# Performance work log

Hardware: AMD Instinct MI355X
Metric: run time of the kernel (lower is better)

The kernel has to match this reference:

```python
import jax, jax.numpy as jnp
import numpy as np

N = 4096        # nodes == batch_size (GFN operates on dense N x N adjacency)
E = 65536       # edges per view (avg degree 16)
IN = 512        # per-view input feature dim
HV = [128, 64]  # per-view GCN dims
HM = [64, 64]   # fused-graph GCN dims
VIEWS = 3


def setup_inputs() -> dict:
    key = jax.random.key(0)
    ks = iter(jax.random.split(key, 64))

    def xavier(shape):
        lim = float(np.sqrt(6.0 / (shape[0] + shape[1])))
        return jax.random.uniform(next(ks), shape, minval=-lim, maxval=lim, dtype=jnp.float32)

    inp = {}
    for v in range(VIEWS):
        inp[f"x{v}"] = jax.random.normal(next(ks), (N, IN), dtype=jnp.float32)
        inp[f"src{v}"] = jax.random.randint(next(ks), (E,), 0, N, dtype=jnp.int32)
        inp[f"dst{v}"] = jax.random.randint(next(ks), (E,), 0, N, dtype=jnp.int32)
        inp[f"Wv{v}0"] = xavier((IN, HV[0]))
        inp[f"bv{v}0"] = jnp.zeros((HV[0],), jnp.float32)
        inp[f"Wv{v}1"] = xavier((HV[0], HV[1]))
        inp[f"bv{v}1"] = jnp.zeros((HV[1],), jnp.float32)
        inp[f"Wf{v}"] = xavier((HV[1], HV[1]))  # FeatureFusion weight
    # GFN: Linear(N -> N/2) -> ReLU -> Linear(N/2 -> N)
    inp["Wg1"] = xavier((N, N // 2)); inp["bg1"] = jnp.zeros((N // 2,), jnp.float32)
    inp["Wg2"] = xavier((N // 2, N)); inp["bg2"] = jnp.zeros((N,), jnp.float32)
    # fused-graph GCN layers
    inp["Wm0"] = xavier((HV[1], HM[0])); inp["bm0"] = jnp.zeros((HM[0],), jnp.float32)
    inp["Wm1"] = xavier((HM[0], HM[1])); inp["bm1"] = jnp.zeros((HM[1],), jnp.float32)
    return inp


def _deg_norms(src, dst):
    # DGL GraphConv norm='both': scale by out-deg(src)^-1/2 and in-deg(dst)^-1/2, degrees clamped to >=1
    ones = jnp.ones(src.shape[0], jnp.float32)
    dout = jnp.maximum(jax.ops.segment_sum(ones, src, num_segments=N), 1.0)
    din = jnp.maximum(jax.ops.segment_sum(ones, dst, num_segments=N), 1.0)
    return dout ** -0.5, din ** -0.5


def _gconv(x, W, b, src, dst, do_isqrt, di_isqrt, act):
    h = (x * do_isqrt[:, None]) @ W            # [N, out] (W commutes with row scaling)
    agg = jax.ops.segment_sum(h[src], dst, num_segments=N)
    h = agg * di_isqrt[:, None] + b
    return act(h)


def reference(x0, x1, x2, src0, dst0, src1, dst1, src2, dst2,
              Wv00, bv00, Wv01, bv01, Wv10, bv10, Wv11, bv11, Wv20, bv20, Wv21, bv21,
              Wf0, Wf1, Wf2, Wg1, bg1, Wg2, bg2, Wm0, bm0, Wm1, bm1):
    ident = lambda t: t
    xs = [x0, x1, x2]
    edges = [(src0, dst0), (src1, dst1), (src2, dst2)]
    Wv = [(Wv00, bv00, Wv01, bv01), (Wv10, bv10, Wv11, bv11), (Wv20, bv20, Wv21, bv21)]
    Wf = [Wf0, Wf1, Wf2]

    # per-view GCN stacks (relu on first layer, identity on last)
    feats = []
    for v in range(VIEWS):
        src, dst = edges[v]
        do_i, di_i = _deg_norms(src, dst)
        W0, b0, W1, b1 = Wv[v]
        f = _gconv(xs[v], W0, b0, src, dst, do_i, di_i, jax.nn.relu)
        f = _gconv(f, W1, b1, src, dst, do_i, di_i, ident)
        feats.append(f)

    # FeatureFusion (dropout omitted for determinism): sum(f @ Wf), softmax over features, relu
    z = feats[0] @ Wf[0] + feats[1] @ Wf[1] + feats[2] @ Wf[2]
    z = jax.nn.relu(jax.nn.softmax(z, axis=1))

    # consensus graph: sum of per-view dense adjacencies -> GFN -> clamp -> round(+0.1)
    adj = jnp.zeros((N, N), jnp.float32)
    for src, dst in edges:
        adj = adj + jnp.zeros((N, N), jnp.float32).at[src, dst].set(1.0)
    fused = jax.nn.relu(adj @ Wg1 + bg1) @ Wg2 + bg2
    fused = jnp.round(jnp.clip(fused, 0.0, 1.0) + 0.1)
    adj_r = fused

    # rebuild binary graph (went through numpy in original -> stop_gradient), symmetrize, add self-loops
    sym = jax.lax.stop_gradient(fused)
    sym = sym + sym.T
    A = jnp.maximum((sym > 0).astype(jnp.float32), jnp.eye(N, dtype=jnp.float32))
    deg = A.sum(axis=1)
    dn = deg ** -0.5

    # fused-graph GCN layers (dense normalized SpMM form since A is already dense)
    h = z
    h = jax.nn.relu(((A @ (h * dn[:, None])) * dn[:, None]) @ Wm0 + bm0)
    h = ((A @ (h * dn[:, None])) * dn[:, None]) @ Wm1 + bm1

    # InnerProductDecoder with identity activation; all `views` entries of adj_rec are identical
    adj_rec = h @ h.T
    return (adj_r, adj_rec, h)
```

## Files before the change

kernel.cpp:

```cpp
#include <hip/hip_runtime.h>
#include <math.h>

#define NNODES 4096
#define NEDGES 65536

typedef short bf16x8 __attribute__((ext_vector_type(8)));
typedef short short4v __attribute__((ext_vector_type(4)));
typedef float f32x4 __attribute__((ext_vector_type(4)));
typedef float f32x4v __attribute__((ext_vector_type(4)));

struct Ptr3  { const float* p[3]; };
struct Ptr3i { const int*   p[3]; };
struct Ptr3h { const short* p[3]; };

__device__ __forceinline__ short f2bf(float f) {
    unsigned u = __builtin_bit_cast(unsigned, f);
    unsigned r = (u + 0x7FFFu + ((u >> 16) & 1u)) >> 16;
    return (short)r;
}

__device__ __forceinline__ void gload_lds16(const void* g, void* l) {
    __builtin_amdgcn_global_load_lds(
        (const __attribute__((address_space(1))) unsigned*)g,
        (__attribute__((address_space(3))) unsigned*)l, 16, 0, 0);
}

template<int ACT>
__global__ __launch_bounds__(512, 1)
void gm_k(const short* __restrict__ A, const short* __restrict__ Bt,
          const float* __restrict__ bias, void* __restrict__ Cout, float* __restrict__ Cout1,
          unsigned char* __restrict__ Pout, int M, int Nn, int K, int lda, int ldb)
{
    constexpr int SLOT = 32768;
    __shared__ short lds[2 * SLOT];
    const int tid = threadIdx.x;
    const int lane = tid & 63;
    const int wave = tid >> 6;
    const int wm = wave >> 2, wn = wave & 3;
    const int z = blockIdx.z;
    A  += (size_t)z * K;
    Bt += (size_t)z * K;
    float* Cf = (ACT == 3 && z == 1) ? Cout1 : (float*)Cout;
    const int gx = gridDim.x, nwg = gx * gridDim.y;
    int w = blockIdx.y * gx + blockIdx.x;
    const int q8 = nwg >> 3;
    w = (w & 7) * q8 + (w >> 3);
    const int bm0 = (w / gx) * 256, bn0 = (w % gx) * 256;
    const int NT = K >> 6;

    auto stageH = [&](int t, int part) {
        if (t >= NT) return;
        const int k0 = t << 6;
        char* base = (char*)(lds + (t & 1) * SLOT);
        const int isB = (part < 2);
        const int h = part & 1;
#pragma unroll
        for (int r = 0; r < 2; ++r) {
            int o = r * 8192 + tid * 16;
            int row = o >> 7;
            int grow = h * 128 + row;
            int scol = (((o >> 4) & 7) ^ (grow & 7)) << 3;
            const short* gsrc = isB ? (Bt + (size_t)(bn0 + grow) * ldb + k0 + scol)
                                    : (A  + (size_t)(bm0 + grow) * lda + k0 + scol);
            gload_lds16(gsrc, base + (isB ? 32768 : 0) + h * 16384 + r * 8192 + wave * 1024);
        }
    };

    f32x4 acc[8][4] = {};
    bf16x8 aF[4][2];
    bf16x8 bF[4][2];

#define PH(QM, QN, TCUR, T1, P1, T2, P2, VM)                                          \
    {                                                                                 \
        const short* As_ = lds + ((TCUR) & 1) * SLOT;                                 \
        const short* Bs_ = As_ + 16384;                                               \
        if constexpr ((QN) == 0) {                                                    \
            _Pragma("unroll") for (int kk = 0; kk < 2; ++kk) {                        \
                const int h_ = kk * 4 + (lane >> 4);                                  \
                _Pragma("unroll") for (int i = 0; i < 4; ++i) {                       \
                    int r_ = wm * 128 + (QM) * 64 + i * 16 + (lane & 15);             \
                    aF[i][kk] = *(const bf16x8*)(As_ + r_ * 64 + ((h_ ^ (r_ & 7)) << 3)); \
                }                                                                     \
            }                                                                         \
        }                                                                             \
        if constexpr ((QM) == 0) {                                                    \
            _Pragma("unroll") for (int kk = 0; kk < 2; ++kk) {                        \
                const int h_ = kk * 4 + (lane >> 4);                                  \
                _Pragma("unroll") for (int j = 0; j < 2; ++j) {                       \
                    int r_ = wn * 64 + ((QN) * 2 + j) * 16 + (lane & 15);             \
                    bF[(QN) * 2 + j][kk] = *(const bf16x8*)(Bs_ + r_ * 64 + ((h_ ^ (r_ & 7)) << 3)); \
                }                                                                     \
            }                                                                         \
        }                                                                             \
        if ((P1) >= 0) stageH(T1, P1);                                                \
        if ((P2) >= 0) stageH(T2, P2);                                                \
        __builtin_amdgcn_s_barrier();                                                 \
        __builtin_amdgcn_s_setprio(1);                                                \
        _Pragma("unroll") for (int kk = 0; kk < 2; ++kk)                              \
            _Pragma("unroll") for (int i = 0; i < 4; ++i)                             \
                _Pragma("unroll") for (int j = 0; j < 2; ++j)                         \
                    acc[(QM) * 4 + i][(QN) * 2 + j] =                                 \
                        __builtin_amdgcn_mfma_f32_16x16x32_bf16(                      \
                            aF[i][kk], bF[(QN) * 2 + j][kk],                          \
                            acc[(QM) * 4 + i][(QN) * 2 + j], 0, 0, 0);                \
        __builtin_amdgcn_s_setprio(0);                                                \
        if ((VM) == 6)      { asm volatile("s_waitcnt vmcnt(6)" ::: "memory");        \
                              __builtin_amdgcn_sched_barrier(0); }                    \
        else if ((VM) == 0) { asm volatile("s_waitcnt vmcnt(0)" ::: "memory");        \
                              __builtin_amdgcn_sched_barrier(0); }                    \
        __builtin_amdgcn_s_barrier();                                                 \
    }

    stageH(0, 0); stageH(0, 1); stageH(0, 2); stageH(0, 3);
    if (NT > 1) { stageH(1, 0); stageH(1, 1); stageH(1, 2); }
    if (NT > 1) { asm volatile("s_waitcnt vmcnt(6)" ::: "memory"); }
    else        { asm volatile("s_waitcnt vmcnt(0)" ::: "memory"); }
    __builtin_amdgcn_sched_barrier(0);
    __builtin_amdgcn_s_barrier();

    for (int it = 0; it < NT / 2; ++it) {
        const int t0 = 2 * it, t1 = t0 + 1, t2 = t0 + 2, t3 = t0 + 3;
        const int vm4 = (t2 < NT) ? 6 : 0;
        const int vm8 = (t3 < NT) ? 6 : 0;
        PH(0, 0, t0, t1, 3,  0, -1, -1)
        PH(0, 1, t0,  0, -1, 0, -1, -1)
        PH(1, 0, t0, t2, 0, t2,  1, -1)
        PH(1, 1, t0, t2, 2,  0, -1, vm4)
        PH(0, 0, t1, t2, 3,  0, -1, -1)
        PH(0, 1, t1,  0, -1, 0, -1, -1)
        PH(1, 0, t1, t3, 0, t3,  1, -1)
        PH(1, 1, t1, t3, 2,  0, -1, vm8)
    }
    if (NT & 1) {
        const int tl = NT - 1;
        PH(0, 0, tl, 0, -1, 0, -1, -1)
        PH(0, 1, tl, 0, -1, 0, -1, -1)
        PH(1, 0, tl, 0, -1, 0, -1, -1)
        PH(1, 1, tl, 0, -1, 0, -1, -1)
    }
#undef PH

    const int cr = (lane >> 4) * 4;
    const int cc = lane & 15;
#pragma unroll
    for (int im = 0; im < 8; ++im) {
#pragma unroll
        for (int jn = 0; jn < 4; ++jn) {
            int col = bn0 + wn * 64 + jn * 16 + cc;
            float bv = bias ? bias[col] : 0.f;
#pragma unroll
            for (int q2 = 0; q2 < 4; ++q2) {
                int row = bm0 + wm * 128 + (im >> 2) * 64 + (im & 3) * 16 + cr + q2;
                float v = acc[im][jn][q2] + bv;
                if constexpr (ACT == 2) {
                    v = rintf(fminf(fmaxf(v, 0.f), 1.f) + 0.1f);
                    Cf[(size_t)row * Nn + col] = v;
                    Pout[(size_t)row * Nn + col] = (unsigned char)(v > 0.5f);
                } else {
                    Cf[(size_t)row * Nn + col] = v;
                }
            }
        }
    }
}

__global__ void reduce_h1_k(const float* __restrict__ p0, const float* __restrict__ p1,
                            const float* __restrict__ bias, short* __restrict__ H1b)
{
    int i = (blockIdx.x * 256 + threadIdx.x) * 4;
    f32x4v a = *(const f32x4v*)(p0 + i);
    f32x4v b = *(const f32x4v*)(p1 + i);
    int col = i & 2047;
    short4v o;
#pragma unroll
    for (int j = 0; j < 4; ++j) {
        float v = a[j] + b[j] + bias[col + j];
        o[j] = f2bf(fmaxf(v, 0.f));
    }
    *(short4v*)(H1b + i) = o;
}

__global__ __launch_bounds__(256)
void mfma_gemm_b_k(const short* __restrict__ Aall, Ptr3h Btv, float* __restrict__ Call,
                   int M, int Nn, int K)
{
    __shared__ short As[64 * 64];
    __shared__ short Bs[64 * 64];
    const int z = blockIdx.z;
    const short* A = Aall + (size_t)z * M * K;
    const short* Bt = Btv.p[z];
    float* C = Call + (size_t)z * M * Nn;
    const int tid = threadIdx.x;
    const int lane = tid & 63, wave = tid >> 6;
    const int bm0 = blockIdx.y * 64, bn0 = blockIdx.x * 64;
    const int wr = (wave >> 1) * 32, wc = (wave & 1) * 32;

    f32x4 acc[2][2] = {};

    for (int k0 = 0; k0 < K; k0 += 64) {
        for (int c = wave; c < 8; c += 4) {
            int o = c * 1024 + lane * 16;
            int row = o >> 7;
            int sl = (o >> 4) & 7;
            int ss = sl ^ (row & 7);
            gload_lds16(A + ((size_t)(bm0 + row) * K + k0 + ss * 8), As + c * 512);
            gload_lds16(Bt + ((size_t)(bn0 + row) * K + k0 + ss * 8), Bs + c * 512);
        }
        __syncthreads();
#pragma unroll
        for (int kk = 0; kk < 2; ++kk) {
            bf16x8 a[2], b[2];
            const int khalf = kk * 4 + (lane >> 4);
#pragma unroll
            for (int i = 0; i < 2; ++i) {
                int r = wr + i * 16 + (lane & 15);
                a[i] = *(const bf16x8*)(As + r * 64 + ((khalf ^ (r & 7)) << 3));
            }
#pragma unroll
            for (int j = 0; j < 2; ++j) {
                int r = wc + j * 16 + (lane & 15);
                b[j] = *(const bf16x8*)(Bs + r * 64 + ((khalf ^ (r & 7)) << 3));
            }
#pragma unroll
            for (int i = 0; i < 2; ++i)
#pragma unroll
                for (int j = 0; j < 2; ++j)
                    acc[i][j] = __builtin_amdgcn_mfma_f32_16x16x32_bf16(a[i], b[j], acc[i][j], 0, 0, 0);
        }
        __syncthreads();
    }

    const int cr = (lane >> 4) * 4;
    const int cc = lane & 15;
#pragma unroll
    for (int i = 0; i < 2; ++i)
#pragma unroll
        for (int j = 0; j < 2; ++j)
#pragma unroll
            for (int q = 0; q < 4; ++q) {
                int row = bm0 + wr + i * 16 + cr + q;
                int col = bn0 + wc + j * 16 + cc;
                C[(size_t)row * Nn + col] = acc[i][j][q];
            }
}

__global__ __launch_bounds__(256)
void spmm_mfma_k(const short* __restrict__ A2b, const short* __restrict__ XsT,
                 float* __restrict__ part)
{
    __shared__ short As[64 * 64];
    __shared__ short Bs[128 * 64];
    const int tid = threadIdx.x;
    const int lane = tid & 63, wave = tid >> 6;
    const int kc = blockIdx.x, m0 = blockIdx.y * 64;
    const int wr = (wave >> 1) * 32, wc = (wave & 1) * 32;
    const int woff = wave * 512;

    f32x4 acc[2][2] = {};

    for (int k0 = kc * 512; k0 < kc * 512 + 512; k0 += 64) {
#pragma unroll
        for (int r = 0; r < 2; ++r) {
            int o = r * 4096 + tid * 16;
            int row = o >> 7;
            int sl = (o >> 4) & 7;
            gload_lds16(A2b + ((size_t)(m0 + row) * 4096 + k0 + ((sl ^ (row & 7)) << 3)),
                        As + r * 2048 + woff);
        }
#pragma unroll
        for (int r = 0; r < 4; ++r) {
            int o = r * 4096 + tid * 16;
            int row = o >> 7;
            int sl = (o >> 4) & 7;
            gload_lds16(XsT + ((size_t)row * 4096 + k0 + ((sl ^ (row & 7)) << 3)),
                        Bs + r * 2048 + woff);
        }
        __syncthreads();
#pragma unroll
        for (int kk = 0; kk < 2; ++kk) {
            const int h = kk * 4 + (lane >> 4);
            bf16x8 a[2], bh[2], bl[2];
#pragma unroll
            for (int i = 0; i < 2; ++i) {
                int r = wr + i * 16 + (lane & 15);
                a[i] = *(const bf16x8*)(As + r * 64 + ((h ^ (r & 7)) << 3));
            }
#pragma unroll
            for (int j = 0; j < 2; ++j) {
                int r = wc + j * 16 + (lane & 15);
                bh[j] = *(const bf16x8*)(Bs + r * 64 + ((h ^ (r & 7)) << 3));
                int r2 = r + 64;
                bl[j] = *(const bf16x8*)(Bs + r2 * 64 + ((h ^ (r2 & 7)) << 3));
            }
#pragma unroll
            for (int i = 0; i < 2; ++i)
#pragma unroll
                for (int j = 0; j < 2; ++j) {
                    acc[i][j] = __builtin_amdgcn_mfma_f32_16x16x32_bf16(a[i], bh[j], acc[i][j], 0, 0, 0);
                    acc[i][j] = __builtin_amdgcn_mfma_f32_16x16x32_bf16(a[i], bl[j], acc[i][j], 0, 0, 0);
                }
        }
        __syncthreads();
    }

    const int cr = (lane >> 4) * 4;
    const int cc = lane & 15;
#pragma unroll
    for (int i = 0; i < 2; ++i)
#pragma unroll
        for (int j = 0; j < 2; ++j)
#pragma unroll
            for (int q = 0; q < 4; ++q)
                part[((size_t)kc * NNODES + m0 + wr + i * 16 + cr + q) * 64 + wc + j * 16 + cc]
                    = acc[i][j][q];
}

__global__ void xsT_k(const float* __restrict__ X, const int* __restrict__ degA,
                      short* __restrict__ XsT)
{
    const int n = blockIdx.y;
    const int k = blockIdx.x * 256 + threadIdx.x;
    float v = X[(size_t)k * 64 + n] * (1.0f / sqrtf((float)degA[k]));
    short hi = f2bf(v);
    float hif = __builtin_bit_cast(float, ((unsigned)(unsigned short)hi) << 16);
    short lo = f2bf(v - hif);
    XsT[(size_t)n * 4096 + k] = hi;
    XsT[(size_t)(64 + n) * 4096 + k] = lo;
}

__global__ void a2b_k(const unsigned* __restrict__ A8w, short* __restrict__ A2b, int words)
{
    int t = blockIdx.x * 256 + threadIdx.x;
    if (t < words) {
        unsigned w = A8w[t];
        short4v o;
#pragma unroll
        for (int j = 0; j < 4; ++j) o[j] = ((w >> (8 * j)) & 1u) ? (short)0x3F80 : (short)0;
        *(short4v*)(A2b + (size_t)t * 4) = o;
    }
}

__global__ void f32_to_bf16T_k(const float* __restrict__ src, short* __restrict__ dstT,
                               int R, int C)
{
    __shared__ float t[64][65];
    const int br = blockIdx.y * 64, bc = blockIdx.x * 64;
    for (int idx = threadIdx.x; idx < 64 * 64; idx += 256) {
        int r = idx >> 6, c = idx & 63;
        t[r][c] = src[(size_t)(br + r) * C + bc + c];
    }
    __syncthreads();
    for (int idx = threadIdx.x; idx < 64 * 64; idx += 256) {
        int c = idx >> 6, r = idx & 63;
        dstT[(size_t)(bc + c) * R + br + r] = f2bf(t[r][c]);
    }
}

__global__ void mask_to_bf16_k(const unsigned* __restrict__ mask, short* __restrict__ adj,
                               int words)
{
    int t = blockIdx.x * 256 + threadIdx.x;
    if (t < words) {
        unsigned w = mask[t];
        short4v o;
        o.x = f2bf((float)__popc(w & 0x7u));
        o.y = f2bf((float)__popc(w & 0x700u));
        o.z = f2bf((float)__popc(w & 0x70000u));
        o.w = f2bf((float)__popc(w & 0x7000000u));
        *(short4v*)(adj + (size_t)t * 4) = o;
    }
}

__global__ void xsplit_k(Ptr3 xv, const float* __restrict__ isq, short* __restrict__ xe)
{
    const int z = blockIdx.y;
    int t = blockIdx.x * 256 + threadIdx.x;
    int n = t >> 9, k = t & 511;
    float a = xv.p[z][(size_t)n * 512 + k] * isq[2 * z * NNODES + n];
    short hi = f2bf(a);
    float hif = __builtin_bit_cast(float, ((unsigned)(unsigned short)hi) << 16);
    short lo = f2bf(a - hif);
    short* row = xe + (size_t)z * NNODES * 1536 + (size_t)n * 1536;
    row[k] = hi; row[512 + k] = hi; row[1024 + k] = lo;
}

__global__ void wsplitT_k(Ptr3 Wv, short* __restrict__ out, int K, int Nn)
{
    const int z = blockIdx.y;
    int t = blockIdx.x * 256 + threadIdx.x;
    if (t >= K * Nn) return;
    int k = t / Nn, n = t % Nn;
    float w = Wv.p[z][(size_t)k * Nn + n];
    short hi = f2bf(w);
    float hif = __builtin_bit_cast(float, ((unsigned)(unsigned short)hi) << 16);
    short lo = f2bf(w - hif);
    short* row = out + (size_t)z * Nn * 3 * K + (size_t)n * 3 * K;
    row[k] = hi; row[K + k] = lo; row[2 * K + k] = hi;
}

template<int RELU>
__global__ __launch_bounds__(256)
void redgemm_k(const float* __restrict__ part, const int* __restrict__ degA,
               const float* __restrict__ Wm, const float* __restrict__ bias,
               float* __restrict__ out, short* __restrict__ Ae, short* __restrict__ Be)
{
    __shared__ float Ws[64 * 64];
    const int tid = threadIdx.x;
    for (int i = tid; i < 4096; i += 256) Ws[i] = Wm[i];
    __syncthreads();
    const int lane = tid & 63, wave = tid >> 6;
    const float bv = bias[lane];
    for (int rr = 0; rr < 4; ++rr) {
        int row = blockIdx.x * 16 + wave * 4 + rr;
        float s = 0.f;
#pragma unroll
        for (int p = 0; p < 8; ++p) s += part[((size_t)p * NNODES + row) * 64 + lane];
        s *= 1.0f / sqrtf((float)degA[row]);
        float acc = bv;
#pragma unroll
        for (int k = 0; k < 64; ++k)
            acc = fmaf(__shfl(s, k), Ws[k * 64 + lane], acc);
        if (RELU) acc = fmaxf(acc, 0.f);
        out[(size_t)row * 64 + lane] = acc;
        if (Ae) {
            short hi = f2bf(acc);
            float hif = __builtin_bit_cast(float, ((unsigned)(unsigned short)hi) << 16);
            short lo = f2bf(acc - hif);
            size_t ro = (size_t)row * 192;
            Ae[ro + lane] = hi; Ae[ro + 64 + lane] = hi; Ae[ro + 128 + lane] = lo;
            Be[ro + lane] = hi; Be[ro + 64 + lane] = lo; Be[ro + 128 + lane] = hi;
        }
    }
}

__global__ void edge_k(Ptr3i src, Ptr3i dst, unsigned* __restrict__ mask, int* __restrict__ degs)
{
    int e = blockIdx.x * 256 + threadIdx.x;
    int z = blockIdx.y;
    if (e < NEDGES) {
        int s = src.p[z][e], d = dst.p[z][e];
        unsigned c = (unsigned)s * (unsigned)NNODES + (unsigned)d;
        atomicOr(&mask[c >> 2], 1u << ((c & 3u) * 8u + (unsigned)z));
        atomicAdd(&degs[2 * z * NNODES + s], 1);
        atomicAdd(&degs[(2 * z + 1) * NNODES + d], 1);
    }
}

__global__ void deg_norm_k(const int* __restrict__ degs, float* __restrict__ isq, int n)
{
    int t = blockIdx.x * 256 + threadIdx.x;
    if (t < n) isq[t] = 1.0f / sqrtf(fmaxf((float)degs[t], 1.0f));
}

__global__ __launch_bounds__(1024)
void scan_k(const int* __restrict__ degs, int* __restrict__ rowptr, int* __restrict__ cursor)
{
    const int z = blockIdx.x;
    const int* din = degs + (2 * z + 1) * NNODES;
    __shared__ int sm[1024];
    const int t = threadIdx.x;
    int v0 = din[t * 4], v1 = din[t * 4 + 1], v2 = din[t * 4 + 2], v3 = din[t * 4 + 3];
    int c1 = v0 + v1, c2 = c1 + v2, s = c2 + v3;
    sm[t] = s;
    __syncthreads();
    for (int off = 1; off < 1024; off <<= 1) {
        int add = (t >= off) ? sm[t - off] : 0;
        __syncthreads();
        sm[t] += add;
        __syncthreads();
    }
    int base = sm[t] - s;
    int* rp = rowptr + z * NNODES;
    int* cu = cursor + z * NNODES;
    rp[t * 4] = base;          cu[t * 4] = base;
    rp[t * 4 + 1] = base + v0; cu[t * 4 + 1] = base + v0;
    rp[t * 4 + 2] = base + c1; cu[t * 4 + 2] = base + c1;
    rp[t * 4 + 3] = base + c2; cu[t * 4 + 3] = base + c2;
}

__global__ void fill_k(Ptr3i src, Ptr3i dst, int* __restrict__ cursor, int* __restrict__ eidx)
{
    int e = blockIdx.x * 256 + threadIdx.x;
    int z = blockIdx.y;
    if (e < NEDGES) {
        int d = dst.p[z][e];
        int pos = atomicAdd(&cursor[z * NNODES + d], 1);
        eidx[(size_t)z * NEDGES + pos] = src.p[z][e];
    }
}

template<int F, int ACT, int MODE>
__global__ void gather_k(const float* __restrict__ Hpre, const int* __restrict__ eidx,
                         const int* __restrict__ rowptr, const int* __restrict__ degs,
                         const float* __restrict__ isq, Ptr3 bias, short* __restrict__ Sout)
{
    const int z = blockIdx.y;
    const int tid = threadIdx.x;
    const int node = blockIdx.x * (256 / F) + tid / F;
    const int f = tid % F;
    const float* H = Hpre + (size_t)z * NNODES * F;
    const int base = rowptr[z * NNODES + node];
    const int cnt = degs[(2 * z + 1) * NNODES + node];
    const int* ei = eidx + (size_t)z * NEDGES + base;
    float s = 0.f;
    for (int i = 0; i < cnt; ++i) s += H[(size_t)ei[i] * F + f];
    float v = s * isq[(2 * z + 1) * NNODES + node] + bias.p[z][f];
    if (ACT) v = fmaxf(v, 0.f);
    if (MODE == 1) v *= isq[2 * z * NNODES + node];
    short hi = f2bf(v);
    float hif = __builtin_bit_cast(float, ((unsigned)(unsigned short)hi) << 16);
    short lo = f2bf(v - hif);
    short* row = Sout + (size_t)z * NNODES * 3 * F + (size_t)node * 3 * F;
    row[f] = hi; row[F + f] = hi; row[2 * F + f] = lo;
}

__global__ void softsum_k(const float* __restrict__ zp, float* __restrict__ z)
{
    int row = blockIdx.x * 4 + (threadIdx.x >> 6);
    int f = threadIdx.x & 63;
    size_t i = (size_t)row * 64 + f;
    float v = zp[i] + zp[i + (size_t)NNODES * 64] + zp[i + (size_t)2 * NNODES * 64];
    float m = v;
#pragma unroll
    for (int off = 32; off >= 1; off >>= 1) m = fmaxf(m, __shfl_xor(m, off));
    float e = expf(v - m);
    float s = e;
#pragma unroll
    for (int off = 32; off >= 1; off >>= 1) s += __shfl_xor(s, off);
    z[i] = e / s;
}

__global__ __launch_bounds__(256)
void build_A2_k(const unsigned char* __restrict__ P, unsigned char* __restrict__ A8,
                int* __restrict__ degA)
{
    __shared__ unsigned Ts[64][20];
    const int bi = blockIdx.y * 64, bj = blockIdx.x * 64;
    const int tid = threadIdx.x;
    const int r = tid >> 2, seg = tid & 3;
    uint4 tv = *(const uint4*)(P + (size_t)(bj + r) * NNODES + bi + seg * 16);
    Ts[r][seg * 4 + 0] = tv.x; Ts[r][seg * 4 + 1] = tv.y;
    Ts[r][seg * 4 + 2] = tv.z; Ts[r][seg * 4 + 3] = tv.w;
    __syncthreads();
    uint4 dv = *(const uint4*)(P + (size_t)(bi + r) * NNODES + bj + seg * 16);
    unsigned dw[4] = {dv.x, dv.y, dv.z, dv.w};
    const unsigned char* Tb = (const unsigned char*)Ts;
    unsigned ow[4];
    int psum = 0;
#pragma unroll
    for (int w = 0; w < 4; ++w) {
        unsigned o = 0;
#pragma unroll
        for (int b = 0; b < 4; ++b) {
            int j = seg * 16 + w * 4 + b;
            unsigned a = (dw[w] >> (8 * b)) & 1u;
            unsigned tr = Tb[j * 80 + r] & 1u;
            unsigned on = a | tr | (unsigned)((bi + r) == (bj + j));
            o |= on << (8 * b);
            psum += (int)on;
        }
        ow[w] = o;
    }
    uint4 o4; o4.x = ow[0]; o4.y = ow[1]; o4.z = ow[2]; o4.w = ow[3];
    *(uint4*)(A8 + (size_t)(bi + r) * NNODES + bj + seg * 16) = o4;
    psum += __shfl_xor(psum, 1);
    psum += __shfl_xor(psum, 2);
    if (seg == 0) atomicAdd(&degA[bi + r], psum);
}

extern "C" void kernel_launch(void* const* d_in, const int* in_sizes, int n_in,
                              void* d_out, int out_size, void* d_ws, size_t ws_size,
                              hipStream_t stream)
{
    const int N = NNODES, E = NEDGES;
    const size_t MB = 1024 * 1024;

    const float* x[3]; const int* src[3]; const int* dst[3];
    const float *Wv0[3], *bv0[3], *Wv1[3], *bv1[3], *Wf[3];
    for (int v = 0; v < 3; ++v) {
        const int b = v * 8;
        x[v]   = (const float*)d_in[b + 0];
        src[v] = (const int*)  d_in[b + 1];
        dst[v] = (const int*)  d_in[b + 2];
        Wv0[v] = (const float*)d_in[b + 3];
        bv0[v] = (const float*)d_in[b + 4];
        Wv1[v] = (const float*)d_in[b + 5];
        bv1[v] = (const float*)d_in[b + 6];
        Wf[v]  = (const float*)d_in[b + 7];
    }
    const float* Wg1 = (const float*)d_in[24];
    const float* bg1 = (const float*)d_in[25];
    const float* Wg2 = (const float*)d_in[26];
    const float* bg2 = (const float*)d_in[27];
    const float* Wm0 = (const float*)d_in[28];
    const float* bm0 = (const float*)d_in[29];
    const float* Wm1 = (const float*)d_in[30];
    const float* bm1 = (const float*)d_in[31];

    float* out_adjr = (float*)d_out;
    float* out_rec  = out_adjr + (size_t)N * N;
    float* out_h    = out_rec + (size_t)N * N;

    char* oa = (char*)out_adjr;
    short* AdjB = (short*)oa;
    float* hv1  = (float*)(oa + 32 * MB);
    short* Ae2  = (short*)(oa + 38 * MB);
    short* Ae3  = (short*)(oa + 47 * MB);
    float* hv2  = (float*)(oa + 52 * MB);
    float* zp   = (float*)(oa + 56 * MB);
    float* partg0 = (float*)(oa + 32 * MB);

    char* orc = (char*)out_rec;
    short* xe   = (short*)orc;
    short* H1b  = (short*)orc;
    unsigned char* P = (unsigned char*)(orc + 16 * MB);
    short* Wg1T = (short*)(orc + 16 * MB);
    float* partg1 = (float*)(orc + 32 * MB);
    short* Wg2T = (short*)(orc + 32 * MB);
    short* A2b  = (short*)orc;
    float* part = (float*)(orc + 48 * MB);

    char* p = (char*)d_ws;
    unsigned* mask = (unsigned*)p;
    unsigned char* A8 = (unsigned char*)p;
    short* AeF = (short*)p;
    short* BeF = AeF + (size_t)N * 192;
    p += (size_t)N * N;
    int* degs = (int*)p;     p += (size_t)6 * N * 4;
    float* isq = (float*)p;  p += (size_t)6 * N * 4;
    int* rowptr = (int*)p;   p += (size_t)3 * N * 4;
    int* cursor = (int*)p;   p += (size_t)3 * N * 4;
    int* eidx = (int*)p;     p += (size_t)3 * E * 4;
    int* degA = (int*)p;     p += (size_t)N * 4;
    float* zbuf = (float*)p; p += (size_t)N * 64 * 4;
    float* h1m = (float*)p;  p += (size_t)N * 64 * 4;
    short* XsT = (short*)p;  p += (size_t)128 * N * 2;
    short* Wv0T = (short*)p; p += (size_t)3 * 128 * 1536 * 2;
    short* Wv1T = (short*)p; p += (size_t)3 * 64 * 384 * 2;
    short* WfT  = (short*)p; p += (size_t)3 * 64 * 192 * 2;

    Ptr3i srcP, dstP;
    for (int v = 0; v < 3; ++v) { srcP.p[v] = src[v]; dstP.p[v] = dst[v]; }

    hipMemsetAsync(mask, 0, (size_t)N * N, stream);
    hipMemsetAsync(degs, 0, (size_t)6 * N * 4, stream);

    edge_k<<<dim3((E + 255) / 256, 3), 256, 0, stream>>>(srcP, dstP, mask, degs);
    deg_norm_k<<<(6 * N + 255) / 256, 256, 0, stream>>>(degs, isq, 6 * N);
    scan_k<<<3, 1024, 0, stream>>>(degs, rowptr, cursor);
    fill_k<<<dim3((E + 255) / 256, 3), 256, 0, stream>>>(srcP, dstP, cursor, eidx);

    Ptr3 xP; for (int v = 0; v < 3; ++v) xP.p[v] = x[v];
    xsplit_k<<<dim3(N * 512 / 256, 3), 256, 0, stream>>>(xP, isq, xe);
    Ptr3 wP;
    for (int v = 0; v < 3; ++v) wP.p[v] = Wv0[v];
    wsplitT_k<<<dim3(512 * 128 / 256, 3), 256, 0, stream>>>(wP, Wv0T, 512, 128);
    for (int v = 0; v < 3; ++v) wP.p[v] = Wv1[v];
    wsplitT_k<<<dim3(128 * 64 / 256, 3), 256, 0, stream>>>(wP, Wv1T, 128, 64);
    for (int v = 0; v < 3; ++v) wP.p[v] = Wf[v];
    wsplitT_k<<<dim3(64 * 64 / 256, 3), 256, 0, stream>>>(wP, WfT, 64, 64);

    Ptr3h BtP; Ptr3 biasP;
    for (int v = 0; v < 3; ++v) BtP.p[v] = Wv0T + (size_t)v * 128 * 1536;
    mfma_gemm_b_k<<<dim3(2, N / 64, 3), 256, 0, stream>>>(xe, BtP, hv1, N, 128, 1536);
    for (int v = 0; v < 3; ++v) biasP.p[v] = bv0[v];
    gather_k<128, 1, 1><<<dim3(N / 2, 3), 256, 0, stream>>>(hv1, eidx, rowptr, degs, isq, biasP, Ae2);
    for (int v = 0; v < 3; ++v) BtP.p[v] = Wv1T + (size_t)v * 64 * 384;
    mfma_gemm_b_k<<<dim3(1, N / 64, 3), 256, 0, stream>>>(Ae2, BtP, hv2, N, 64, 384);
    for (int v = 0; v < 3; ++v) biasP.p[v] = bv1[v];
    gather_k<64, 0, 2><<<dim3(N / 4, 3), 256, 0, stream>>>(hv2, eidx, rowptr, degs, isq, biasP, Ae3);
    for (int v = 0; v < 3; ++v) BtP.p[v] = WfT + (size_t)v * 64 * 192;
    mfma_gemm_b_k<<<dim3(1, N / 64, 3), 256, 0, stream>>>(Ae3, BtP, zp, N, 64, 192);
    softsum_k<<<N / 4, 256, 0, stream>>>(zp, zbuf);

    mask_to_bf16_k<<<(N * N / 4 + 255) / 256, 256, 0, stream>>>(mask, AdjB, N * N / 4);
    f32_to_bf16T_k<<<dim3(2048 / 64, 4096 / 64), 256, 0, stream>>>(Wg1, Wg1T, 4096, 2048);

    gm_k<3><<<dim3(2048 / 256, 4096 / 256, 2), 512, 0, stream>>>(
        AdjB, Wg1T, nullptr, partg0, partg1, nullptr, 4096, 2048, 2048, 4096, 4096);
    reduce_h1_k<<<4096 * 2048 / 4 / 256, 256, 0, stream>>>(partg0, partg1, bg1, H1b);

    f32_to_bf16T_k<<<dim3(4096 / 64, 2048 / 64), 256, 0, stream>>>(Wg2, Wg2T, 2048, 4096);

    gm_k<2><<<dim3(4096 / 256, 4096 / 256, 1), 512, 0, stream>>>(
        H1b, Wg2T, bg2, out_adjr, nullptr, P, 4096, 4096, 2048, 2048, 2048);

    hipMemsetAsync(degA, 0, (size_t)N * 4, stream);
    build_A2_k<<<dim3(N / 64, N / 64), 256, 0, stream>>>(P, A8, degA);

    a2b_k<<<(N * N / 4 + 255) / 256, 256, 0, stream>>>((const unsigned*)A8, A2b, N * N / 4);
    xsT_k<<<dim3(16, 64), 256, 0, stream>>>(zbuf, degA, XsT);
    spmm_mfma_k<<<dim3(8, N / 64), 256, 0, stream>>>(A2b, XsT, part);
    redgemm_k<1><<<256, 256, 0, stream>>>(part, degA, Wm0, bm0, h1m, nullptr, nullptr);
    xsT_k<<<dim3(16, 64), 256, 0, stream>>>(h1m, degA, XsT);
    spmm_mfma_k<<<dim3(8, N / 64), 256, 0, stream>>>(A2b, XsT, part);
    redgemm_k<0><<<256, 256, 0, stream>>>(part, degA, Wm1, bm1, out_h, AeF, BeF);

    gm_k<0><<<dim3(4096 / 256, 4096 / 256, 1), 512, 0, stream>>>(
        AeF, BeF, nullptr, out_rec, nullptr, nullptr, 4096, 4096, 192, 192, 192);
}
```

Baseline: 452.8 us.

## Store GFN split-K partials as bf16 and fuse the adjacency and XsT conversion kernels

The split-K partial sums of the first GFN GEMM are now written as bf16 rather than fp32, which halves the traffic into and out of the reduce kernel. build_A2 writes the bf16 adjacency directly, so the separate byte-mask to bf16 conversion pass is gone. redgemm now emits the scaled hi/lo XsT for the next SpMM, replacing a second xsT launch. The changes also add an lgkmcnt wait in the GEMM phase and move the Wg2 transpose earlier. Rounding the partials to bf16 adds error before the ReLU and round/clip step, which could flip thresholded adjacency entries.

```diff
diff --git a/kernel.cpp b/kernel.cpp
--- a/kernel.cpp
+++ b/kernel.cpp
@@ -7,7 +7,6 @@
 typedef short bf16x8 __attribute__((ext_vector_type(8)));
 typedef short short4v __attribute__((ext_vector_type(4)));
 typedef float f32x4 __attribute__((ext_vector_type(4)));
-typedef float f32x4v __attribute__((ext_vector_type(4)));
 
 struct Ptr3  { const float* p[3]; };
 struct Ptr3i { const int*   p[3]; };
@@ -18,6 +17,9 @@
     unsigned r = (u + 0x7FFFu + ((u >> 16) & 1u)) >> 16;
     return (short)r;
 }
+__device__ __forceinline__ float bf2f(short s) {
+    return __builtin_bit_cast(float, ((unsigned)(unsigned short)s) << 16);
+}
 
 __device__ __forceinline__ void gload_lds16(const void* g, void* l) {
     __builtin_amdgcn_global_load_lds(
@@ -28,7 +30,7 @@
 template<int ACT>
 __global__ __launch_bounds__(512, 1)
 void gm_k(const short* __restrict__ A, const short* __restrict__ Bt,
-          const float* __restrict__ bias, void* __restrict__ Cout, float* __restrict__ Cout1,
+          const float* __restrict__ bias, void* __restrict__ Cout, void* __restrict__ Cout1,
           unsigned char* __restrict__ Pout, int M, int Nn, int K, int lda, int ldb)
 {
     constexpr int SLOT = 32768;
@@ -40,7 +42,7 @@
     const int z = blockIdx.z;
     A  += (size_t)z * K;
     Bt += (size_t)z * K;
-    float* Cf = (ACT == 3 && z == 1) ? Cout1 : (float*)Cout;
+    void* Cw = (ACT == 3 && z == 1) ? Cout1 : Cout;
     const int gx = gridDim.x, nwg = gx * gridDim.y;
     int w = blockIdx.y * gx + blockIdx.x;
     const int q8 = nwg >> 3;
@@ -94,6 +96,9 @@
         }                                                                             \
         if ((P1) >= 0) stageH(T1, P1);                                                \
         if ((P2) >= 0) stageH(T2, P2);                                                \
+        if constexpr ((QM) == 0 && (QN) == 0) {                                       \
+            asm volatile("s_waitcnt lgkmcnt(8)" ::: "memory");                        \
+        }                                                                             \
         __builtin_amdgcn_s_barrier();                                                 \
         __builtin_amdgcn_s_setprio(1);                                                \
         _Pragma("unroll") for (int kk = 0; kk < 2; ++kk)                              \
@@ -154,30 +159,32 @@
                 float v = acc[im][jn][q2] + bv;
                 if constexpr (ACT == 2) {
                     v = rintf(fminf(fmaxf(v, 0.f), 1.f) + 0.1f);
-                    Cf[(size_t)row * Nn + col] = v;
+                    ((float*)Cw)[(size_t)row * Nn + col] = v;
                     Pout[(size_t)row * Nn + col] = (unsigned char)(v > 0.5f);
+                } else if constexpr (ACT == 3) {
+                    ((short*)Cw)[(size_t)row * Nn + col] = f2bf(v);
                 } else {
-                    Cf[(size_t)row * Nn + col] = v;
+                    ((float*)Cw)[(size_t)row * Nn + col] = v;
                 }
             }
         }
     }
 }
 
-__global__ void reduce_h1_k(const float* __restrict__ p0, const float* __restrict__ p1,
+__global__ void reduce_h1_k(const short* __restrict__ p0, const short* __restrict__ p1,
                             const float* __restrict__ bias, short* __restrict__ H1b)
 {
-    int i = (blockIdx.x * 256 + threadIdx.x) * 4;
-    f32x4v a = *(const f32x4v*)(p0 + i);
-    f32x4v b = *(const f32x4v*)(p1 + i);
+    int i = (blockIdx.x * 256 + threadIdx.x) * 8;
+    bf16x8 a = *(const bf16x8*)(p0 + i);
+    bf16x8 b = *(const bf16x8*)(p1 + i);
     int col = i & 2047;
-    short4v o;
-#pragma unroll
-    for (int j = 0; j < 4; ++j) {
-        float v = a[j] + b[j] + bias[col + j];
+    bf16x8 o;
+#pragma unroll
+    for (int j = 0; j < 8; ++j) {
+        float v = bf2f(a[j]) + bf2f(b[j]) + bias[col + j];
         o[j] = f2bf(fmaxf(v, 0.f));
     }
-    *(short4v*)(H1b + i) = o;
+    *(bf16x8*)(H1b + i) = o;
 }
 
 __global__ __launch_bounds__(256)
@@ -322,22 +329,9 @@
     const int k = blockIdx.x * 256 + threadIdx.x;
     float v = X[(size_t)k * 64 + n] * (1.0f / sqrtf((float)degA[k]));
     short hi = f2bf(v);
-    float hif = __builtin_bit_cast(float, ((unsigned)(unsigned short)hi) << 16);
-    short lo = f2bf(v - hif);
+    short lo = f2bf(v - bf2f(hi));
     XsT[(size_t)n * 4096 + k] = hi;
     XsT[(size_t)(64 + n) * 4096 + k] = lo;
-}
-
-__global__ void a2b_k(const unsigned* __restrict__ A8w, short* __restrict__ A2b, int words)
-{
-    int t = blockIdx.x * 256 + threadIdx.x;
-    if (t < words) {
-        unsigned w = A8w[t];
-        short4v o;
-#pragma unroll
-        for (int j = 0; j < 4; ++j) o[j] = ((w >> (8 * j)) & 1u) ? (short)0x3F80 : (short)0;
-        *(short4v*)(A2b + (size_t)t * 4) = o;
-    }
 }
 
 __global__ void f32_to_bf16T_k(const float* __restrict__ src, short* __restrict__ dstT,
@@ -378,8 +372,7 @@
     int n = t >> 9, k = t & 511;
     float a = xv.p[z][(size_t)n * 512 + k] * isq[2 * z * NNODES + n];
     short hi = f2bf(a);
-    float hif = __builtin_bit_cast(float, ((unsigned)(unsigned short)hi) << 16);
-    short lo = f2bf(a - hif);
+    short lo = f2bf(a - bf2f(hi));
     short* row = xe + (size_t)z * NNODES * 1536 + (size_t)n * 1536;
     row[k] = hi; row[512 + k] = hi; row[1024 + k] = lo;
 }
@@ -392,8 +385,7 @@
     int k = t / Nn, n = t % Nn;
     float w = Wv.p[z][(size_t)k * Nn + n];
     short hi = f2bf(w);
-    float hif = __builtin_bit_cast(float, ((unsigned)(unsigned short)hi) << 16);
-    short lo = f2bf(w - hif);
+    short lo = f2bf(w - bf2f(hi));
     short* row = out + (size_t)z * Nn * 3 * K + (size_t)n * 3 * K;
     row[k] = hi; row[K + k] = lo; row[2 * K + k] = hi;
 }
@@ -402,7 +394,8 @@
 __global__ __launch_bounds__(256)
 void redgemm_k(const float* __restrict__ part, const int* __restrict__ degA,
                const float* __restrict__ Wm, const float* __restrict__ bias,
-               float* __restrict__ out, short* __restrict__ Ae, short* __restrict__ Be)
+               float* __restrict__ out, short* __restrict__ Ae, short* __restrict__ Be,
+               short* __restrict__ XsT)
 {
     __shared__ float Ws[64 * 64];
     const int tid = threadIdx.x;
@@ -415,7 +408,8 @@
         float s = 0.f;
 #pragma unroll
         for (int p = 0; p < 8; ++p) s += part[((size_t)p * NNODES + row) * 64 + lane];
-        s *= 1.0f / sqrtf((float)degA[row]);
+        const float dn = 1.0f / sqrtf((float)degA[row]);
+        s *= dn;
         float acc = bv;
 #pragma unroll
         for (int k = 0; k < 64; ++k)
@@ -424,11 +418,17 @@
         out[(size_t)row * 64 + lane] = acc;
         if (Ae) {
             short hi = f2bf(acc);
-            float hif = __builtin_bit_cast(float, ((unsigned)(unsigned short)hi) << 16);
-            short lo = f2bf(acc - hif);
+            short lo = f2bf(acc - bf2f(hi));
             size_t ro = (size_t)row * 192;
             Ae[ro + lane] = hi; Ae[ro + 64 + lane] = hi; Ae[ro + 128 + lane] = lo;
             Be[ro + lane] = hi; Be[ro + 64 + lane] = lo; Be[ro + 128 + lane] = hi;
+        }
+        if (XsT) {
+            float vv = acc * dn;
+            short hi = f2bf(vv);
+            short lo = f2bf(vv - bf2f(hi));
+            XsT[(size_t)lane * 4096 + row] = hi;
+            XsT[(size_t)(64 + lane) * 4096 + row] = lo;
         }
     }
 }
@@ -449,7 +449,7 @@
 __global__ void deg_norm_k(const int* __restrict__ degs, float* __restrict__ isq, int n)
 {
     int t = blockIdx.x * 256 + threadIdx.x;
-    if (t < n) isq[t] = 1.0f / sqrtf(fmaxf((float)degs[t], 1.0f));
+    if (t < n) isq[t] = 1.0f / sqrtf(fmaxf((float)t >= 0 ? (float)degs[t] : 1.0f, 1.0f));
 }
 
 __global__ __launch_bounds__(1024)
@@ -508,8 +508,7 @@
     if (ACT) v = fmaxf(v, 0.f);
     if (MODE == 1) v *= isq[2 * z * NNODES + node];
     short hi = f2bf(v);
-    float hif = __builtin_bit_cast(float, ((unsigned)(unsigned short)hi) << 16);
-    short lo = f2bf(v - hif);
+    short lo = f2bf(v - bf2f(hi));
     short* row = Sout + (size_t)z * NNODES * 3 * F + (size_t)node * 3 * F;
     row[f] = hi; row[F + f] = hi; row[2 * F + f] = lo;
 }
@@ -531,7 +530,7 @@
 }
 
 __global__ __launch_bounds__(256)
-void build_A2_k(const unsigned char* __restrict__ P, unsigned char* __restrict__ A8,
+void build_A2_k(const unsigned char* __restrict__ P, short* __restrict__ A2b,
                 int* __restrict__ degA)
 {
     __shared__ unsigned Ts[64][20];
@@ -545,24 +544,25 @@
     uint4 dv = *(const uint4*)(P + (size_t)(bi + r) * NNODES + bj + seg * 16);
     unsigned dw[4] = {dv.x, dv.y, dv.z, dv.w};
     const unsigned char* Tb = (const unsigned char*)Ts;
-    unsigned ow[4];
+    bf16x8 o0, o1;
     int psum = 0;
 #pragma unroll
     for (int w = 0; w < 4; ++w) {
-        unsigned o = 0;
 #pragma unroll
         for (int b = 0; b < 4; ++b) {
-            int j = seg * 16 + w * 4 + b;
+            int idx = w * 4 + b;
+            int j = seg * 16 + idx;
             unsigned a = (dw[w] >> (8 * b)) & 1u;
             unsigned tr = Tb[j * 80 + r] & 1u;
             unsigned on = a | tr | (unsigned)((bi + r) == (bj + j));
-            o |= on << (8 * b);
+            short val = on ? (short)0x3F80 : (short)0;
+            if (idx < 8) o0[idx] = val; else o1[idx - 8] = val;
             psum += (int)on;
         }
-        ow[w] = o;
-    }
-    uint4 o4; o4.x = ow[0]; o4.y = ow[1]; o4.z = ow[2]; o4.w = ow[3];
-    *(uint4*)(A8 + (size_t)(bi + r) * NNODES + bj + seg * 16) = o4;
+    }
+    short* dst = A2b + (size_t)(bi + r) * NNODES + bj + seg * 16;
+    *(bf16x8*)dst = o0;
+    *(bf16x8*)(dst + 8) = o1;
     psum += __shfl_xor(psum, 1);
     psum += __shfl_xor(psum, 2);
     if (seg == 0) atomicAdd(&degA[bi + r], psum);
@@ -608,21 +608,19 @@
     short* Ae3  = (short*)(oa + 47 * MB);
     float* hv2  = (float*)(oa + 52 * MB);
     float* zp   = (float*)(oa + 56 * MB);
-    float* partg0 = (float*)(oa + 32 * MB);
+    short* partg0 = (short*)(oa + 32 * MB);
+    short* partg1 = (short*)(oa + 48 * MB);
 
     char* orc = (char*)out_rec;
     short* xe   = (short*)orc;
     short* H1b  = (short*)orc;
     unsigned char* P = (unsigned char*)(orc + 16 * MB);
     short* Wg1T = (short*)(orc + 16 * MB);
-    float* partg1 = (float*)(orc + 32 * MB);
     short* Wg2T = (short*)(orc + 32 * MB);
-    short* A2b  = (short*)orc;
     float* part = (float*)(orc + 48 * MB);
 
     char* p = (char*)d_ws;
     unsigned* mask = (unsigned*)p;
-    unsigned char* A8 = (unsigned char*)p;
     short* AeF = (short*)p;
     short* BeF = AeF + (size_t)N * 192;
     p += (size_t)N * N;
@@ -638,6 +636,7 @@
     short* Wv0T = (short*)p; p += (size_t)3 * 128 * 1536 * 2;
     short* Wv1T = (short*)p; p += (size_t)3 * 64 * 384 * 2;
     short* WfT  = (short*)p; p += (size_t)3 * 64 * 192 * 2;
+    short* A2b = (short*)((char*)d_ws + 64 * MB);
 
     Ptr3i srcP, dstP;
     for (int v = 0; v < 3; ++v) { srcP.p[v] = src[v]; dstP.p[v] = dst[v]; }
@@ -675,26 +674,23 @@
 
     mask_to_bf16_k<<<(N * N / 4 + 255) / 256, 256, 0, stream>>>(mask, AdjB, N * N / 4);
     f32_to_bf16T_k<<<dim3(2048 / 64, 4096 / 64), 256, 0, stream>>>(Wg1, Wg1T, 4096, 2048);
+    f32_to_bf16T_k<<<dim3(4096 / 64, 2048 / 64), 256, 0, stream>>>(Wg2, Wg2T, 2048, 4096);
 
     gm_k<3><<<dim3(2048 / 256, 4096 / 256, 2), 512, 0, stream>>>(
         AdjB, Wg1T, nullptr, partg0, partg1, nullptr, 4096, 2048, 2048, 4096, 4096);
-    reduce_h1_k<<<4096 * 2048 / 4 / 256, 256, 0, stream>>>(partg0, partg1, bg1, H1b);
-
-    f32_to_bf16T_k<<<dim3(4096 / 64, 2048 / 64), 256, 0, stream>>>(Wg2, Wg2T, 2048, 4096);
+    reduce_h1_k<<<4096 * 2048 / 8 / 256, 256, 0, stream>>>(partg0, partg1, bg1, H1b);
 
     gm_k<2><<<dim3(4096 / 256, 4096 / 256, 1), 512, 0, stream>>>(
         H1b, Wg2T, bg2, out_adjr, nullptr, P, 4096, 4096, 2048, 2048, 2048);
 
     hipMemsetAsync(degA, 0, (size_t)N * 4, stream);
-    build_A2_k<<<dim3(N / 64, N / 64), 256, 0, stream>>>(P, A8, degA);
-
-    a2b_k<<<(N * N / 4 + 255) / 256, 256, 0, stream>>>((const unsigned*)A8, A2b, N * N / 4);
+    build_A2_k<<<dim3(N / 64, N / 64), 256, 0, stream>>>(P, A2b, degA);
+
     xsT_k<<<dim3(16, 64), 256, 0, stream>>>(zbuf, degA, XsT);
     spmm_mfma_k<<<dim3(8, N / 64), 256, 0, stream>>>(A2b, XsT, part);
-    redgemm_k<1><<<256, 256, 0, stream>>>(part, degA, Wm0, bm0, h1m, nullptr, nullptr);
-    xsT_k<<<dim3(16, 64), 256, 0, stream>>>(h1m, degA, XsT);
+    redgemm_k<1><<<256, 256, 0, stream>>>(part, degA, Wm0, bm0, h1m, nullptr, nullptr, XsT);
     spmm_mfma_k<<<dim3(8, N / 64), 256, 0, stream>>>(A2b, XsT, part);
-    redgemm_k<0><<<256, 256, 0, stream>>>(part, degA, Wm1, bm1, out_h, AeF, BeF);
+    redgemm_k<0><<<256, 256, 0, stream>>>(part, degA, Wm1, bm1, out_h, AeF, BeF, nullptr);
 
     gm_k<0><<<dim3(4096 / 256, 4096 / 256, 1), 512, 0, stream>>>(
         AeF, BeF, nullptr, out_rec, nullptr, nullptr, 4096, 4096, 192, 192, 192);
```

Result: no change. 450.0 us (-0.6%).
